# Kernel tuning notes

Hardware: AMD Instinct MI355X
Metric: run time of the kernel (lower is better)

Reference implementation:

```python
import jax, jax.numpy as jnp
import numpy as np

NUM_CLASSES = 91
DELTA = 1.0


def _safe_div(num, den):
    # tf.math.divide_no_nan semantics
    return jnp.where(den != 0, num / jnp.where(den != 0, den, 1.0), 0.0)


def setup_inputs() -> dict:
    key = jax.random.key(0)
    k1, k2, k3, k4 = jax.random.split(key, 4)
    B, R, C = 32, 2048, NUM_CLASSES
    class_outputs = jax.random.normal(k1, (B, R, C), dtype=jnp.float32)
    box_outputs = jax.random.normal(k2, (B, R, C * 4), dtype=jnp.float32)
    class_targets = jax.random.randint(k3, (B, R), 0, C, dtype=jnp.int32)
    box_targets = jax.random.normal(k4, (B, R, 4), dtype=jnp.float32)
    return {
        "class_outputs": class_outputs,
        "box_outputs": box_outputs,
        "class_targets": class_targets,
        "box_targets": box_targets,
    }


def reference(class_outputs, box_outputs, class_targets, box_targets):
    B, R, C = class_outputs.shape

    # --- box selection: gather the per-RoI box for the target class ---
    # (the original emulates this gather with a giant one-hot matmul)
    box = box_outputs.reshape(B, R, C, 4)
    sel = jnp.take_along_axis(
        box, class_targets[:, :, None, None].astype(jnp.int32), axis=2
    )[:, :, 0, :]  # [B, R, 4]

    # --- box loss: Huber (smooth L1) on positive RoIs only ---
    mask = jnp.broadcast_to((class_targets > 0)[:, :, None], sel.shape)  # [B,R,4]
    mask_f = mask.astype(jnp.float32)
    diff = box_targets - sel
    absd = jnp.abs(diff)
    huber = jnp.where(absd <= DELTA, 0.5 * diff * diff, DELTA * (absd - 0.5 * DELTA))
    num_non_zeros = jnp.sum(mask_f)
    box_loss = _safe_div(jnp.sum(huber * mask_f), num_non_zeros)

    # --- class loss: softmax cross-entropy averaged over nonzero one-hot entries ---
    onehot = jax.nn.one_hot(class_targets, C, dtype=jnp.float32)  # [B,R,C]
    logsm = jax.nn.log_softmax(class_outputs, axis=-1)
    ce = -jnp.sum(onehot * logsm, axis=-1)  # [B,R]
    n_labels = jnp.sum((onehot != 0).astype(jnp.float32))
    class_loss = _safe_div(jnp.sum(ce), n_labels)

    return class_loss, box_loss
```

## Files before the change

kernel.cpp:

```cpp
#include <hip/hip_runtime.h>
#include <math.h>

#define NC 91
#define NROWS 65536
#define ROWS_PER_BLK 32
#define NBLK (NROWS / ROWS_PER_BLK)
#define TPB 128
#define TILE_FLOATS (ROWS_PER_BLK * NC)
#define TILE_F4 (TILE_FLOATS / 4)

__global__ __launch_bounds__(TPB) void frcnn_main(
    const float* __restrict__ cls, const float* __restrict__ box,
    const int* __restrict__ tgt, const float* __restrict__ btgt,
    float4* __restrict__ partial)
{
    __shared__ float lds[TILE_FLOATS];
    __shared__ float s_ce[2], s_h[2], s_c[2];

    const int tid = threadIdx.x;
    const int blk = blockIdx.x;

    const float4* src = (const float4*)cls + (size_t)blk * TILE_F4;
    float4* dst = (float4*)lds;
    #pragma unroll
    for (int k = 0; k < 6; ++k) {
        int idx = tid + k * TPB;
        if (idx < TILE_F4) dst[idx] = src[idx];
    }

    const int row  = tid >> 2;
    const int q    = tid & 3;
    const int grow = blk * ROWS_PER_BLK + row;

    const int   t  = tgt[grow];
    const float bo = box[((size_t)grow * NC + t) * 4 + q];
    const float bt = btgt[(size_t)grow * 4 + q];

    float hub = 0.f, cn = 0.f;
    {
        float d  = bt - bo;
        float ad = fabsf(d);
        float h  = (ad <= 1.f) ? 0.5f * d * d : ad - 0.5f;
        if (t > 0) { hub = h; cn = 1.f; }
    }

    __syncthreads();

    const int ei = q * 23;
    const float* myrow = lds + row * NC;
    float a0 = 0.f, a1 = 0.f, a2 = 0.f, a3 = 0.f;
    #pragma unroll
    for (int j = 0; j < 20; j += 4) {
        a0 += __expf(myrow[ei + j]);
        a1 += __expf(myrow[ei + j + 1]);
        a2 += __expf(myrow[ei + j + 2]);
        a3 += __expf(myrow[ei + j + 3]);
    }
    a0 += __expf(myrow[ei + 20]);
    a1 += __expf(myrow[ei + 21]);
    if (q != 3) a2 += __expf(myrow[ei + 22]);

    float e = (a0 + a1) + (a2 + a3);
    e += __shfl_xor(e, 1);
    e += __shfl_xor(e, 2);

    float ce_s = 0.f;
    if (q == 0) ce_s = __logf(e) - myrow[t];

    #pragma unroll
    for (int off = 32; off; off >>= 1) {
        ce_s += __shfl_xor(ce_s, off);
        hub  += __shfl_xor(hub,  off);
        cn   += __shfl_xor(cn,   off);
    }

    const int wid  = tid >> 6;
    const int lane = tid & 63;
    if (lane == 0) { s_ce[wid] = ce_s; s_h[wid] = hub; s_c[wid] = cn; }
    __syncthreads();
    if (tid == 0) {
        float tce = s_ce[0] + s_ce[1];
        float th  = s_h[0]  + s_h[1];
        float tc  = s_c[0]  + s_c[1];
        partial[blk] = make_float4(tce, th, tc, 0.f);
    }
}

__global__ __launch_bounds__(256) void frcnn_finalize(
    const float4* __restrict__ part, float* __restrict__ out)
{
    const int tid = threadIdx.x;
    double ce = 0.0, h = 0.0, c = 0.0;
    #pragma unroll
    for (int k = 0; k < 8; ++k) {
        float4 p = part[tid + k * 256];
        ce += (double)p.x; h += (double)p.y; c += (double)p.z;
    }
    #pragma unroll
    for (int off = 32; off; off >>= 1) {
        ce += __shfl_xor(ce, off);
        h  += __shfl_xor(h,  off);
        c  += __shfl_xor(c,  off);
    }
    __shared__ double s[12];
    const int wid = tid >> 6, lane = tid & 63;
    if (lane == 0) { s[wid * 3] = ce; s[wid * 3 + 1] = h; s[wid * 3 + 2] = c; }
    __syncthreads();
    if (tid == 0) {
        double tce = 0.0, th = 0.0, tc = 0.0;
        #pragma unroll
        for (int i = 0; i < 4; ++i) { tce += s[i*3]; th += s[i*3+1]; tc += s[i*3+2]; }
        out[0] = (float)(tce / (double)NROWS);
        out[1] = (float)(tc != 0.0 ? th / tc : 0.0);
    }
}

extern "C" void kernel_launch(void* const* d_in, const int* in_sizes, int n_in,
                              void* d_out, int out_size, void* d_ws, size_t ws_size,
                              hipStream_t stream)
{
    const float* cls  = (const float*)d_in[0];
    const float* box  = (const float*)d_in[1];
    const int*   tgt  = (const int*)d_in[2];
    const float* btgt = (const float*)d_in[3];
    float*  out  = (float*)d_out;
    float4* part = (float4*)d_ws;

    frcnn_main<<<NBLK, TPB, 0, stream>>>(cls, box, tgt, btgt, part);
    frcnn_finalize<<<1, 256, 0, stream>>>(part, out);
}
```

Before: 12.81 us.

## Fuse finalize reduction into main kernel via flag-based last-block spin

Removes the separate finalize launch. Each block publishes its partial sums with a release-stored magic flag, and the last block spins on every slot's flag before reducing all partials in double precision and resetting the flags. This saves one kernel launch and the inter-kernel gap. It risks deadlock if the last block is scheduled before the others can make progress, and it relies on the workspace flags starting cleared. The spin-waiting also adds serialized latency at the tail.

```diff
diff --git a/kernel.cpp b/kernel.cpp
--- a/kernel.cpp
+++ b/kernel.cpp
@@ -8,11 +8,12 @@
 #define TPB 128
 #define TILE_FLOATS (ROWS_PER_BLK * NC)
 #define TILE_F4 (TILE_FLOATS / 4)
+#define MAGIC 0x5EC7A11Fu
 
-__global__ __launch_bounds__(TPB) void frcnn_main(
+__global__ __launch_bounds__(TPB) void frcnn_fused(
     const float* __restrict__ cls, const float* __restrict__ box,
     const int* __restrict__ tgt, const float* __restrict__ btgt,
-    float4* __restrict__ partial)
+    float4* __restrict__ part, float* __restrict__ out)
 {
     __shared__ float lds[TILE_FLOATS];
     __shared__ float s_ce[2], s_h[2], s_c[2];
@@ -78,40 +79,46 @@
     const int lane = tid & 63;
     if (lane == 0) { s_ce[wid] = ce_s; s_h[wid] = hub; s_c[wid] = cn; }
     __syncthreads();
+
     if (tid == 0) {
         float tce = s_ce[0] + s_ce[1];
         float th  = s_h[0]  + s_h[1];
         float tc  = s_c[0]  + s_c[1];
-        partial[blk] = make_float4(tce, th, tc, 0.f);
+        unsigned* slot = (unsigned*)(part + blk);
+        __hip_atomic_store(slot + 0, __float_as_uint(tce), __ATOMIC_RELAXED, __HIP_MEMORY_SCOPE_AGENT);
+        __hip_atomic_store(slot + 1, __float_as_uint(th),  __ATOMIC_RELAXED, __HIP_MEMORY_SCOPE_AGENT);
+        __hip_atomic_store(slot + 2, __float_as_uint(tc),  __ATOMIC_RELAXED, __HIP_MEMORY_SCOPE_AGENT);
+        __hip_atomic_store(slot + 3, MAGIC,                __ATOMIC_RELEASE, __HIP_MEMORY_SCOPE_AGENT);
     }
-}
 
-__global__ __launch_bounds__(256) void frcnn_finalize(
-    const float4* __restrict__ part, float* __restrict__ out)
-{
-    const int tid = threadIdx.x;
-    double ce = 0.0, h = 0.0, c = 0.0;
-    #pragma unroll
-    for (int k = 0; k < 8; ++k) {
-        float4 p = part[tid + k * 256];
-        ce += (double)p.x; h += (double)p.y; c += (double)p.z;
-    }
-    #pragma unroll
-    for (int off = 32; off; off >>= 1) {
-        ce += __shfl_xor(ce, off);
-        h  += __shfl_xor(h,  off);
-        c  += __shfl_xor(c,  off);
-    }
-    __shared__ double s[12];
-    const int wid = tid >> 6, lane = tid & 63;
-    if (lane == 0) { s[wid * 3] = ce; s[wid * 3 + 1] = h; s[wid * 3 + 2] = c; }
-    __syncthreads();
-    if (tid == 0) {
-        double tce = 0.0, th = 0.0, tc = 0.0;
+    if (blk == NBLK - 1) {
+        double ce = 0.0, h = 0.0, c = 0.0;
         #pragma unroll
-        for (int i = 0; i < 4; ++i) { tce += s[i*3]; th += s[i*3+1]; tc += s[i*3+2]; }
-        out[0] = (float)(tce / (double)NROWS);
-        out[1] = (float)(tc != 0.0 ? th / tc : 0.0);
+        for (int k = 0; k < NBLK / TPB; ++k) {
+            const int s = tid + k * TPB;
+            unsigned* sl = (unsigned*)(part + s);
+            while (__hip_atomic_load(sl + 3, __ATOMIC_ACQUIRE, __HIP_MEMORY_SCOPE_AGENT) != MAGIC) { }
+            ce += (double)__uint_as_float(__hip_atomic_load(sl + 0, __ATOMIC_RELAXED, __HIP_MEMORY_SCOPE_AGENT));
+            h  += (double)__uint_as_float(__hip_atomic_load(sl + 1, __ATOMIC_RELAXED, __HIP_MEMORY_SCOPE_AGENT));
+            c  += (double)__uint_as_float(__hip_atomic_load(sl + 2, __ATOMIC_RELAXED, __HIP_MEMORY_SCOPE_AGENT));
+            __hip_atomic_store(sl + 3, 0u, __ATOMIC_RELAXED, __HIP_MEMORY_SCOPE_AGENT);
+        }
+        #pragma unroll
+        for (int off = 32; off; off >>= 1) {
+            ce += __shfl_xor(ce, off);
+            h  += __shfl_xor(h,  off);
+            c  += __shfl_xor(c,  off);
+        }
+        __shared__ double sd[6];
+        if (lane == 0) { sd[wid * 3] = ce; sd[wid * 3 + 1] = h; sd[wid * 3 + 2] = c; }
+        __syncthreads();
+        if (tid == 0) {
+            double tce = sd[0] + sd[3];
+            double th  = sd[1] + sd[4];
+            double tc  = sd[2] + sd[5];
+            out[0] = (float)(tce / (double)NROWS);
+            out[1] = (float)(tc != 0.0 ? th / tc : 0.0);
+        }
     }
 }
 
@@ -126,6 +133,5 @@
     float*  out  = (float*)d_out;
     float4* part = (float4*)d_ws;
 
-    frcnn_main<<<NBLK, TPB, 0, stream>>>(cls, box, tgt, btgt, part);
-    frcnn_finalize<<<1, 256, 0, stream>>>(part, out);
+    frcnn_fused<<<NBLK, TPB, 0, stream>>>(cls, box, tgt, btgt, part, out);
 }
```

After: 31.51 us. +146.0%, slower.
